# Performance work log

Hardware: AMD Instinct MI355X
Metric: run time of the kernel (lower is better)

Reference implementation:

```python
import jax, jax.numpy as jnp
import numpy as np

MODEL_DIM = 1024
H = 16
DK = MODEL_DIM // H


def setup_inputs() -> dict:
    key = jax.random.key(0)
    ks = jax.random.split(key, 11)
    B, S, D = 4, 2048, MODEL_DIM
    s = 1.0 / np.sqrt(D)
    inp = {
        "q": jax.random.normal(ks[0], (B, S, D), jnp.float32),
        "k": jax.random.normal(ks[1], (B, S, D), jnp.float32),
        "v": jax.random.normal(ks[2], (B, S, D), jnp.float32),
        # stacked per-head projection weights [H, D, DK] and biases [H, DK]
        "wq_w": jax.random.normal(ks[3], (H, D, DK), jnp.float32) * s,
        "wq_b": jax.random.normal(ks[4], (H, DK), jnp.float32) * s,
        "wk_w": jax.random.normal(ks[5], (H, D, DK), jnp.float32) * s,
        "wk_b": jax.random.normal(ks[6], (H, DK), jnp.float32) * s,
        "wv_w": jax.random.normal(ks[7], (H, D, DK), jnp.float32) * s,
        "wv_b": jax.random.normal(ks[8], (H, DK), jnp.float32) * s,
        "wo_w": jax.random.normal(ks[9], (D, D), jnp.float32) * s,
        "wo_b": jax.random.normal(ks[10], (D,), jnp.float32) * s,
    }
    return inp


def reference(q, k, v, wq_w, wq_b, wk_w, wk_b, wv_w, wv_b, wo_w, wo_b):
    # per-head projections, batched over heads: [B,S,D] x [H,D,DK] -> [B,H,S,DK]
    qh = jnp.einsum('bsd,hdk->bhsk', q, wq_w) + wq_b[None, :, None, :]
    kh = jnp.einsum('bsd,hdk->bhsk', k, wk_w) + wk_b[None, :, None, :]
    vh = jnp.einsum('bsd,hdk->bhsk', v, wv_w) + wv_b[None, :, None, :]
    scale = 1.0 / jnp.sqrt(jnp.asarray(DK, qh.dtype))
    scores = jnp.einsum('bhqk,bhsk->bhqs', qh, kh) * scale  # [B,H,S,S]
    out = jnp.einsum('bhqs,bhsk->bhqk', scores, vh)         # [B,H,S,DK]
    # NON-STANDARD: softmax applied AFTER the value matmul, over last dim (dv)
    out = jax.nn.softmax(out, axis=-1)
    # concat heads along feature dim: [B,S,H*DK]
    B, Hh, S, Dk = out.shape
    heads = jnp.transpose(out, (0, 2, 1, 3)).reshape(B, S, Hh * Dk)
    return heads @ wo_w.T + wo_b
```

## Files before the change

### kernel.cpp

```cpp
#include <hip/hip_runtime.h>
#include <math.h>

#define B 4
#define S 2048
#define D 1024
#define H 16
#define DK 64
#define MS (B * S)
#define GKA 2048

typedef short bf16x8 __attribute__((ext_vector_type(8)));
typedef float f32x4 __attribute__((ext_vector_type(4)));

__device__ __forceinline__ unsigned short f2bf(float x) {
  union { float f; unsigned u; } v; v.f = x;
  unsigned r = v.u + 0x7fff + ((v.u >> 16) & 1);
  return (unsigned short)(r >> 16);
}
__device__ __forceinline__ float bf2f(unsigned short h) {
  union { unsigned u; float f; } v; v.u = ((unsigned)h) << 16;
  return v.f;
}
__device__ __forceinline__ void split2(float x, unsigned short& hi, unsigned short& lo) {
  hi = f2bf(x);
  lo = f2bf(x - bf2f(hi));
}

__global__ __launch_bounds__(256) void prep_kernel(
    const float* __restrict__ q, const float* __restrict__ k, const float* __restrict__ v,
    const float* __restrict__ wk, const float* __restrict__ wv, const float* __restrict__ wq,
    const float* __restrict__ wo,
    unsigned short* __restrict__ KSP, unsigned short* __restrict__ VSP,
    unsigned short* __restrict__ QSP,
    unsigned short* __restrict__ WKS, unsigned short* __restrict__ WVS,
    unsigned short* __restrict__ WQA, unsigned short* __restrict__ WOB,
    float* __restrict__ M) {
  const int blk = blockIdx.x;
  const int tid = threadIdx.x;
  if (blk < 24576) {
    const int which = blk >> 13;
    const int bb = blk & 8191;
    const float* X = which == 0 ? k : (which == 1 ? v : q);
    unsigned short* O = which == 0 ? KSP : (which == 1 ? VSP : QSP);
    int t = bb * 256 + tid;
    int idx = t * 4;
    int m = idx >> 10, d = idx & 1023;
    float4 x = *(const float4*)&X[idx];
    union { unsigned short h[4]; ushort4 u; } uh, ul;
    split2(x.x, uh.h[0], ul.h[0]);
    split2(x.y, uh.h[1], ul.h[1]);
    split2(x.z, uh.h[2], ul.h[2]);
    split2(x.w, uh.h[3], ul.h[3]);
    *(ushort4*)&O[(size_t)m * GKA + d] = uh.u;
    *(ushort4*)&O[(size_t)m * GKA + 1024 + d] = ul.u;
  } else if (blk < 32768) {
    const int which = (blk - 24576) >> 12;
    const int bb = (blk - 24576) & 4095;
    const float* W = which == 0 ? wk : wv;
    unsigned short* O = which == 0 ? WKS : WVS;
    int t = bb * 256 + tid;
    int d = t & 1023, n = t >> 10;
    int h = n >> 6, dk = n & 63;
    float x = W[((size_t)(h << 10) + d) * 64 + dk];
    unsigned short hi, lo;
    split2(x, hi, lo);
    size_t ro = (size_t)n * GKA + d;
    O[ro] = hi;
    O[ro + 1024] = lo;
  } else if (blk < 36864) {
    int t = (blk - 32768) * 256 + tid;
    int kk = t & 63;
    int hd = t >> 6;
    float x = wq[t];
    unsigned short hi, lo;
    split2(x, hi, lo);
    WQA[(size_t)hd * 128 + kk] = hi;
    WQA[(size_t)hd * 128 + 64 + kk] = lo;
  } else if (blk < 37888) {
    int t = (blk - 36864) * 256 + tid;
    int idx = t * 4;
    float4 x = *(const float4*)&wo[idx];
    ushort4 u;
    u.x = f2bf(x.x); u.y = f2bf(x.y); u.z = f2bf(x.z); u.w = f2bf(x.w);
    *(ushort4*)&WOB[idx] = u;
  } else {
    int t = (blk - 37888) * 256 + tid;
    *(float4*)&M[(size_t)t * 4] = (float4){0.f, 0.f, 0.f, 0.f};
  }
}

#define BK 32
template <int SPLIT>
__global__ __launch_bounds__(256) void gemm_kernel(
    const unsigned short* __restrict__ A0, const unsigned short* __restrict__ A1,
    const unsigned short* __restrict__ B0, const unsigned short* __restrict__ B1,
    const float* __restrict__ bias0, const float* __restrict__ bias1,
    float* __restrict__ C0, float* __restrict__ C1) {
  const int KLOG = SPLIT ? 3072 : 1024;
  const int AST = SPLIT ? 2048 : 1024;
  const int BST = SPLIT ? 2048 : 1024;
  const unsigned short* A = blockIdx.z ? A1 : A0;
  const unsigned short* BT = blockIdx.z ? B1 : B0;
  const float* bias = blockIdx.z ? bias1 : bias0;
  float* C = blockIdx.z ? C1 : C0;

  __shared__ __align__(16) unsigned short As[128 * BK];
  __shared__ __align__(16) unsigned short Bs[128 * BK];
  const int tid = threadIdx.x;
  const int lane = tid & 63;
  const int w = tid >> 6;
  const int wm = (w >> 1) * 64;
  const int wn = (w & 1) * 64;
  const size_t bm = (size_t)blockIdx.y * 128;
  const size_t bn = (size_t)blockIdx.x * 128;

  f32x4 acc[4][4];
#pragma unroll
  for (int i = 0; i < 4; i++)
#pragma unroll
    for (int j = 0; j < 4; j++) acc[i][j] = (f32x4){0.f, 0.f, 0.f, 0.f};

  const int srow = lane >> 2;
  const int skof = (lane & 3) * 8;
  const unsigned short* Ag0 = A + (bm + w * 32 + srow) * AST + skof;
  const unsigned short* Ag1 = Ag0 + (size_t)16 * AST;
  const unsigned short* Bg0 = BT + (bn + w * 32 + srow) * BST + skof;
  const unsigned short* Bg1 = Bg0 + (size_t)16 * BST;
  unsigned short* As0 = As + (w * 2) * 512;
  unsigned short* As1 = As0 + 512;
  unsigned short* Bs0 = Bs + (w * 2) * 512;
  unsigned short* Bs1 = Bs0 + 512;

  const int fm = lane & 15;
  const int fk = (lane >> 4) * 8;

  for (int k0 = 0; k0 < KLOG; k0 += BK) {
    const int aofs = SPLIT ? (k0 < 2048 ? k0 : k0 - 2048) : k0;
    const int bofs = SPLIT ? (k0 < 1024 ? k0 : k0 - 1024) : k0;
    __syncthreads();
    __builtin_amdgcn_global_load_lds((const __attribute__((address_space(1))) void*)(Ag0 + aofs),
                                     (__attribute__((address_space(3))) void*)As0, 16, 0, 0);
    __builtin_amdgcn_global_load_lds((const __attribute__((address_space(1))) void*)(Ag1 + aofs),
                                     (__attribute__((address_space(3))) void*)As1, 16, 0, 0);
    __builtin_amdgcn_global_load_lds((const __attribute__((address_space(1))) void*)(Bg0 + bofs),
                                     (__attribute__((address_space(3))) void*)Bs0, 16, 0, 0);
    __builtin_amdgcn_global_load_lds((const __attribute__((address_space(1))) void*)(Bg1 + bofs),
                                     (__attribute__((address_space(3))) void*)Bs1, 16, 0, 0);
    __syncthreads();
    bf16x8 af[4], bf[4];
#pragma unroll
    for (int i = 0; i < 4; i++) {
      af[i] = *(const bf16x8*)&As[(wm + i * 16 + fm) * BK + fk];
      bf[i] = *(const bf16x8*)&Bs[(wn + i * 16 + fm) * BK + fk];
    }
#pragma unroll
    for (int i = 0; i < 4; i++)
#pragma unroll
      for (int j = 0; j < 4; j++)
        acc[i][j] = __builtin_amdgcn_mfma_f32_16x16x32_bf16(af[i], bf[j], acc[i][j], 0, 0, 0);
  }

  const int r0 = (lane >> 4) * 4;
#pragma unroll
  for (int i = 0; i < 4; i++)
#pragma unroll
    for (int j = 0; j < 4; j++) {
      size_t row = bm + wm + i * 16 + r0;
      size_t col = bn + wn + j * 16 + fm;
      float bb = bias[col];
#pragma unroll
      for (int r = 0; r < 4; r++) C[(row + r) * D + col] = acc[i][j][r] + bb;
    }
}

__global__ __launch_bounds__(256) void gemm_q_softmax(
    const unsigned short* __restrict__ A, const unsigned short* __restrict__ WQM,
    const float* __restrict__ BQM, unsigned short* __restrict__ HB) {
  const int b = blockIdx.y >> 4;
  const unsigned short* BT = WQM + (size_t)b * D * GKA;

  __shared__ __align__(16) unsigned short As[128 * BK];
  __shared__ __align__(16) unsigned short Bs[128 * BK];
  const int tid = threadIdx.x;
  const int lane = tid & 63;
  const int w = tid >> 6;
  const int wm = (w >> 1) * 64;
  const int wn = (w & 1) * 64;
  const size_t bm = (size_t)blockIdx.y * 128;
  const size_t bn = (size_t)blockIdx.x * 128;

  f32x4 acc[4][4];
#pragma unroll
  for (int i = 0; i < 4; i++)
#pragma unroll
    for (int j = 0; j < 4; j++) acc[i][j] = (f32x4){0.f, 0.f, 0.f, 0.f};

  const int srow = lane >> 2;
  const int skof = (lane & 3) * 8;
  const unsigned short* Ag0 = A + (bm + w * 32 + srow) * GKA + skof;
  const unsigned short* Ag1 = Ag0 + (size_t)16 * GKA;
  const unsigned short* Bg0 = BT + (bn + w * 32 + srow) * GKA + skof;
  const unsigned short* Bg1 = Bg0 + (size_t)16 * GKA;
  unsigned short* As0 = As + (w * 2) * 512;
  unsigned short* As1 = As0 + 512;
  unsigned short* Bs0 = Bs + (w * 2) * 512;
  unsigned short* Bs1 = Bs0 + 512;

  const int fm = lane & 15;
  const int fk = (lane >> 4) * 8;

  for (int k0 = 0; k0 < 3072; k0 += BK) {
    const int aofs = (k0 < 2048) ? k0 : k0 - 2048;
    const int bofs = (k0 < 1024) ? k0 : k0 - 1024;
    __syncthreads();
    __builtin_amdgcn_global_load_lds((const __attribute__((address_space(1))) void*)(Ag0 + aofs),
                                     (__attribute__((address_space(3))) void*)As0, 16, 0, 0);
    __builtin_amdgcn_global_load_lds((const __attribute__((address_space(1))) void*)(Ag1 + aofs),
                                     (__attribute__((address_space(3))) void*)As1, 16, 0, 0);
    __builtin_amdgcn_global_load_lds((const __attribute__((address_space(1))) void*)(Bg0 + bofs),
                                     (__attribute__((address_space(3))) void*)Bs0, 16, 0, 0);
    __builtin_amdgcn_global_load_lds((const __attribute__((address_space(1))) void*)(Bg1 + bofs),
                                     (__attribute__((address_space(3))) void*)Bs1, 16, 0, 0);
    __syncthreads();
    bf16x8 af[4], bf[4];
#pragma unroll
    for (int i = 0; i < 4; i++) {
      af[i] = *(const bf16x8*)&As[(wm + i * 16 + fm) * BK + fk];
      bf[i] = *(const bf16x8*)&Bs[(wn + i * 16 + fm) * BK + fk];
    }
#pragma unroll
    for (int i = 0; i < 4; i++)
#pragma unroll
      for (int j = 0; j < 4; j++)
        acc[i][j] = __builtin_amdgcn_mfma_f32_16x16x32_bf16(af[i], bf[j], acc[i][j], 0, 0, 0);
  }

  const int quad = lane >> 4;
  const size_t head_col0 = bn + wn;
  float bj[4];
#pragma unroll
  for (int j = 0; j < 4; j++) bj[j] = BQM[(size_t)b * D + head_col0 + j * 16 + fm];

#pragma unroll
  for (int i = 0; i < 4; i++) {
    f32x4 val[4];
#pragma unroll
    for (int j = 0; j < 4; j++)
#pragma unroll
      for (int r = 0; r < 4; r++) val[j][r] = (acc[i][j][r] + bj[j]) * 0.125f;

    f32x4 mx = val[0];
#pragma unroll
    for (int j = 1; j < 4; j++)
#pragma unroll
      for (int r = 0; r < 4; r++) mx[r] = fmaxf(mx[r], val[j][r]);
#pragma unroll
    for (int off = 1; off < 16; off <<= 1)
#pragma unroll
      for (int r = 0; r < 4; r++) mx[r] = fmaxf(mx[r], __shfl_xor(mx[r], off, 64));

    f32x4 e[4];
    f32x4 sm = (f32x4){0.f, 0.f, 0.f, 0.f};
#pragma unroll
    for (int j = 0; j < 4; j++)
#pragma unroll
      for (int r = 0; r < 4; r++) {
        e[j][r] = __expf(val[j][r] - mx[r]);
        sm[r] += e[j][r];
      }
#pragma unroll
    for (int off = 1; off < 16; off <<= 1)
#pragma unroll
      for (int r = 0; r < 4; r++) sm[r] += __shfl_xor(sm[r], off, 64);

    f32x4 inv;
#pragma unroll
    for (int r = 0; r < 4; r++) inv[r] = 1.0f / sm[r];

#pragma unroll
    for (int j = 0; j < 4; j++)
#pragma unroll
      for (int r = 0; r < 4; r++) {
        size_t row = bm + wm + i * 16 + quad * 4 + r;
        HB[row * D + head_col0 + j * 16 + fm] = f2bf(e[j][r] * inv[r]);
      }
  }
}

__global__ __launch_bounds__(256) void compute_m_kernel(
    const float* __restrict__ KH, const float* __restrict__ VH, float* __restrict__ Mout) {
  const int sc = blockIdx.x, h = blockIdx.y, b = blockIdx.z;
  const int tid = threadIdx.x;
  const int i0 = (tid >> 4) * 4;
  const int j0 = (tid & 15) * 4;
  __shared__ float ks[16][64], vs[16][64];
  float acc[4][4];
#pragma unroll
  for (int a = 0; a < 4; a++)
#pragma unroll
    for (int c = 0; c < 4; c++) acc[a][c] = 0.f;

  const int s0 = sc * (S / 8);
  const int rr = tid >> 4;
  const int cc = (tid & 15) * 4;
  for (int s = s0; s < s0 + S / 8; s += 16) {
    size_t base = ((size_t)b * S + s + rr) * D + h * 64 + cc;
    __syncthreads();
    *(float4*)&ks[rr][cc] = *(const float4*)&KH[base];
    *(float4*)&vs[rr][cc] = *(const float4*)&VH[base];
    __syncthreads();
#pragma unroll
    for (int ss = 0; ss < 16; ss++) {
      float4 kf = *(const float4*)&ks[ss][i0];
      float4 vf = *(const float4*)&vs[ss][j0];
      float ka[4] = {kf.x, kf.y, kf.z, kf.w};
      float va[4] = {vf.x, vf.y, vf.z, vf.w};
#pragma unroll
      for (int a = 0; a < 4; a++)
#pragma unroll
        for (int c = 0; c < 4; c++) acc[a][c] += ka[a] * va[c];
    }
  }
  float* Mp = Mout + ((size_t)(b * H + h)) * DK * DK;
#pragma unroll
  for (int a = 0; a < 4; a++)
#pragma unroll
    for (int c = 0; c < 4; c++) atomicAdd(&Mp[(i0 + a) * DK + j0 + c], acc[a][c]);
}

__global__ __launch_bounds__(256) void split_m_bias_kernel(
    const float* __restrict__ M, const float* __restrict__ bq,
    unsigned short* __restrict__ MSP, float* __restrict__ BQM) {
  const int bh = blockIdx.x;
  const int h = bh & 15;
  const float* Mp = M + (size_t)bh * 4096;
  unsigned short* hiP = MSP + (size_t)bh * 8192;
  unsigned short* loP = hiP + 4096;
  for (int idx = threadIdx.x; idx < 4096; idx += 256) {
    int kk = idx >> 6, nn = idx & 63;
    unsigned short hi, lo;
    split2(Mp[idx], hi, lo);
    hiP[nn * 64 + kk] = hi;
    loP[nn * 64 + kk] = lo;
  }
  if (threadIdx.x < 64) {
    int j = threadIdx.x;
    float a = 0.f;
#pragma unroll 8
    for (int kk = 0; kk < 64; kk++) a += bq[h * 64 + kk] * Mp[kk * 64 + j];
    BQM[(size_t)bh * 64 + j] = a;
  }
}

__global__ __launch_bounds__(256) void wqm_kernel(
    const unsigned short* __restrict__ WQA, const unsigned short* __restrict__ MSP,
    unsigned short* __restrict__ WQM) {
  const int c = blockIdx.x, h = blockIdx.y, b = blockIdx.z;
  const int tid = threadIdx.x;
  const int lane = tid & 63;
  const int w = tid >> 6;
  const int fm = lane & 15;
  const int quad = lane >> 4;
  const int ko = quad * 8;
  const int dbase = c * 64 + w * 16;

  const unsigned short* arow = WQA + ((size_t)h * 1024 + dbase + fm) * 128;
  bf16x8 ahi0 = *(const bf16x8*)&arow[ko];
  bf16x8 ahi1 = *(const bf16x8*)&arow[32 + ko];
  bf16x8 alo0 = *(const bf16x8*)&arow[64 + ko];
  bf16x8 alo1 = *(const bf16x8*)&arow[96 + ko];

  const unsigned short* hiP = MSP + ((size_t)(b * H + h)) * 8192;
  const unsigned short* loP = hiP + 4096;
  f32x4 acc[4];
#pragma unroll
  for (int j = 0; j < 4; j++) acc[j] = (f32x4){0.f, 0.f, 0.f, 0.f};
#pragma unroll
  for (int j = 0; j < 4; j++) {
    bf16x8 bhi0 = *(const bf16x8*)&hiP[(j * 16 + fm) * 64 + ko];
    bf16x8 bhi1 = *(const bf16x8*)&hiP[(j * 16 + fm) * 64 + 32 + ko];
    bf16x8 blo0 = *(const bf16x8*)&loP[(j * 16 + fm) * 64 + ko];
    bf16x8 blo1 = *(const bf16x8*)&loP[(j * 16 + fm) * 64 + 32 + ko];
    acc[j] = __builtin_amdgcn_mfma_f32_16x16x32_bf16(ahi0, bhi0, acc[j], 0, 0, 0);
    acc[j] = __builtin_amdgcn_mfma_f32_16x16x32_bf16(ahi1, bhi1, acc[j], 0, 0, 0);
    acc[j] = __builtin_amdgcn_mfma_f32_16x16x32_bf16(alo0, bhi0, acc[j], 0, 0, 0);
    acc[j] = __builtin_amdgcn_mfma_f32_16x16x32_bf16(alo1, bhi1, acc[j], 0, 0, 0);
    acc[j] = __builtin_amdgcn_mfma_f32_16x16x32_bf16(ahi0, blo0, acc[j], 0, 0, 0);
    acc[j] = __builtin_amdgcn_mfma_f32_16x16x32_bf16(ahi1, blo1, acc[j], 0, 0, 0);
  }

#pragma unroll
  for (int j = 0; j < 4; j++) {
    int n = h * 64 + j * 16 + fm;
    ushort4 hv, lv;
    unsigned short hi, lo;
    split2(acc[j][0], hi, lo); hv.x = hi; lv.x = lo;
    split2(acc[j][1], hi, lo); hv.y = hi; lv.y = lo;
    split2(acc[j][2], hi, lo); hv.z = hi; lv.z = lo;
    split2(acc[j][3], hi, lo); hv.w = hi; lv.w = lo;
    size_t base = ((size_t)b * D + n) * GKA + dbase + quad * 4;
    *(ushort4*)&WQM[base] = hv;
    *(ushort4*)&WQM[base + 1024] = lv;
  }
}

extern "C" void kernel_launch(void* const* d_in, const int* in_sizes, int n_in,
                              void* d_out, int out_size, void* d_ws, size_t ws_size,
                              hipStream_t stream) {
  const float* q = (const float*)d_in[0];
  const float* k = (const float*)d_in[1];
  const float* v = (const float*)d_in[2];
  const float* wq_w = (const float*)d_in[3];
  const float* wq_b = (const float*)d_in[4];
  const float* wk_w = (const float*)d_in[5];
  const float* wk_b = (const float*)d_in[6];
  const float* wv_w = (const float*)d_in[7];
  const float* wv_b = (const float*)d_in[8];
  const float* wo_w = (const float*)d_in[9];
  const float* wo_b = (const float*)d_in[10];
  float* out = (float*)d_out;

  unsigned short* KSP = (unsigned short*)d_ws;
  unsigned short* VSP = KSP + (size_t)16 * 1024 * 1024;
  unsigned short* QSP = VSP + (size_t)16 * 1024 * 1024;
  float* VH = (float*)(QSP + (size_t)16 * 1024 * 1024);
  float* M = VH + (size_t)MS * D;
  unsigned short* WKS = (unsigned short*)(M + 256 * 1024);
  unsigned short* WVS = WKS + (size_t)2 * 1024 * 1024;
  unsigned short* WQA = WVS + (size_t)2 * 1024 * 1024;
  unsigned short* WOB = WQA + (size_t)2 * 1024 * 1024;
  float* KH = out;
  unsigned short* HB = KSP;
  unsigned short* WQM = KSP + (size_t)8 * 1024 * 1024;
  unsigned short* MSP = VSP;
  float* BQM = (float*)(VSP + 512 * 1024);

  dim3 blk(256);

  prep_kernel<<<38144, blk, 0, stream>>>(q, k, v, wk_w, wv_w, wq_w, wo_w,
                                         KSP, VSP, QSP, WKS, WVS, WQA, WOB, M);
  gemm_kernel<1><<<dim3(8, 64, 2), blk, 0, stream>>>(KSP, VSP, WKS, WVS, wk_b, wv_b, KH, VH);
  compute_m_kernel<<<dim3(8, H, B), blk, 0, stream>>>(KH, VH, M);
  split_m_bias_kernel<<<64, blk, 0, stream>>>(M, wq_b, MSP, BQM);
  wqm_kernel<<<dim3(16, H, B), blk, 0, stream>>>(WQA, MSP, WQM);
  gemm_q_softmax<<<dim3(8, 64), blk, 0, stream>>>(QSP, WQM, BQM, HB);
  gemm_kernel<0><<<dim3(8, 64, 1), blk, 0, stream>>>(HB, HB, WOB, WOB, wo_b, wo_b, out, out);
}
```

Baseline: 480.7 us.

## Replace K/V projection GEMM with 256x256-tile double-buffered direct-to-LDS kernel

Adds a new GEMM kernel for the K and V projections that uses 256x256 output tiles with 512 threads. It double-buffers LDS staging through global_load_lds with an XOR swizzle to avoid bank conflicts, and raises wave priority around the MFMA blocks. The larger tile raises arithmetic intensity and the async loads overlap memory with compute, replacing the previous 128x128 gemm_kernel<1>. The trade-off is large LDS use (128KB per block) and high register pressure from 32 accumulators per lane, which limits occupancy. The 48-step K loop switches its source offset partway through, and that offset logic is easy to get wrong.

```diff
diff --git a/kernel.cpp b/kernel.cpp
--- a/kernel.cpp
+++ b/kernel.cpp
@@ -173,6 +173,126 @@
     }
 }
 
+__device__ __forceinline__ void stage256(
+    const unsigned short* __restrict__ A, const unsigned short* __restrict__ BT,
+    const unsigned* aoffs, const unsigned* boffs,
+    unsigned short* Asb, unsigned short* Bsb, int aof, int bof, int w) {
+#pragma unroll
+  for (int g = 0; g < 4; ++g)
+    __builtin_amdgcn_global_load_lds(
+        (const __attribute__((address_space(1))) void*)(A + aoffs[g] + aof),
+        (__attribute__((address_space(3))) void*)(Asb + g * 4096 + w * 512), 16, 0, 0);
+#pragma unroll
+  for (int g = 0; g < 4; ++g)
+    __builtin_amdgcn_global_load_lds(
+        (const __attribute__((address_space(1))) void*)(BT + boffs[g] + bof),
+        (__attribute__((address_space(3))) void*)(Bsb + g * 4096 + w * 512), 16, 0, 0);
+}
+
+__global__ __launch_bounds__(512, 2) void gemm256_kernel(
+    const unsigned short* __restrict__ A0, const unsigned short* __restrict__ A1,
+    const unsigned short* __restrict__ B0, const unsigned short* __restrict__ B1,
+    const float* __restrict__ bias0, const float* __restrict__ bias1,
+    float* __restrict__ C0, float* __restrict__ C1) {
+  const unsigned short* __restrict__ A = blockIdx.z ? A1 : A0;
+  const unsigned short* __restrict__ BT = blockIdx.z ? B1 : B0;
+  const float* __restrict__ bias = blockIdx.z ? bias1 : bias0;
+  float* __restrict__ C = blockIdx.z ? C1 : C0;
+
+  __shared__ __align__(16) unsigned short As[2][256 * 64];
+  __shared__ __align__(16) unsigned short Bs[2][256 * 64];
+
+  const int tid = threadIdx.x;
+  const int lane = tid & 63;
+  const int w = tid >> 6;
+  const int wr = w >> 2;
+  const int wc = w & 3;
+  const int fm = lane & 15;
+  const int quad = lane >> 4;
+  const int sx = (fm & 7) << 3;
+  const size_t bm = (size_t)blockIdx.y * 256;
+  const size_t bn = (size_t)blockIdx.x * 256;
+
+  const int srow = tid >> 3;
+  const int scol = ((tid & 7) ^ (srow & 7)) << 3;
+  unsigned aoffs[4], boffs[4];
+#pragma unroll
+  for (int g = 0; g < 4; ++g) {
+    aoffs[g] = (unsigned)((bm + g * 64 + srow) * 2048 + scol);
+    boffs[g] = (unsigned)((bn + g * 64 + srow) * 2048 + scol);
+  }
+
+  f32x4 acc[8][4];
+#pragma unroll
+  for (int i = 0; i < 8; ++i)
+#pragma unroll
+    for (int j = 0; j < 4; ++j) acc[i][j] = (f32x4){0.f, 0.f, 0.f, 0.f};
+
+  stage256(A, BT, aoffs, boffs, As[0], Bs[0], 0, 0, w);
+  stage256(A, BT, aoffs, boffs, As[1], Bs[1], 64, 64, w);
+
+  for (int t = 0; t < 48; ++t) {
+    const int cur = t & 1;
+    if (t < 47)
+      asm volatile("s_waitcnt vmcnt(8)" ::: "memory");
+    else
+      asm volatile("s_waitcnt vmcnt(0)" ::: "memory");
+    __builtin_amdgcn_s_barrier();
+    asm volatile("" ::: "memory");
+
+    const unsigned short* Ab = As[cur];
+    const unsigned short* Bb = Bs[cur];
+
+    bf16x8 bfr[4][2];
+#pragma unroll
+    for (int j = 0; j < 4; ++j)
+#pragma unroll
+      for (int kk = 0; kk < 2; ++kk)
+        bfr[j][kk] = *(const bf16x8*)&Bb[((wc * 64 + j * 16 + fm) * 64 + kk * 32 + quad * 8) ^ sx];
+
+#pragma unroll
+    for (int qq = 0; qq < 4; ++qq) {
+      bf16x8 afr[2][2];
+#pragma unroll
+      for (int ii = 0; ii < 2; ++ii)
+#pragma unroll
+        for (int kk = 0; kk < 2; ++kk)
+          afr[ii][kk] = *(const bf16x8*)&Ab[((wr * 128 + (qq * 2 + ii) * 16 + fm) * 64 + kk * 32 + quad * 8) ^ sx];
+      __builtin_amdgcn_s_setprio(1);
+#pragma unroll
+      for (int ii = 0; ii < 2; ++ii)
+#pragma unroll
+        for (int j = 0; j < 4; ++j) {
+          acc[qq * 2 + ii][j] =
+              __builtin_amdgcn_mfma_f32_16x16x32_bf16(afr[ii][0], bfr[j][0], acc[qq * 2 + ii][j], 0, 0, 0);
+          acc[qq * 2 + ii][j] =
+              __builtin_amdgcn_mfma_f32_16x16x32_bf16(afr[ii][1], bfr[j][1], acc[qq * 2 + ii][j], 0, 0, 0);
+        }
+      __builtin_amdgcn_s_setprio(0);
+      __builtin_amdgcn_s_barrier();
+      asm volatile("" ::: "memory");
+    }
+
+    if (t + 2 < 48) {
+      const int k0 = (t + 2) * 64;
+      const int aof = k0 < 2048 ? k0 : k0 - 2048;
+      const int bof = k0 < 1024 ? k0 : k0 - 1024;
+      stage256(A, BT, aoffs, boffs, As[cur], Bs[cur], aof, bof, w);
+    }
+  }
+
+#pragma unroll
+  for (int i = 0; i < 8; ++i)
+#pragma unroll
+    for (int j = 0; j < 4; ++j) {
+      size_t row = bm + wr * 128 + i * 16 + quad * 4;
+      size_t col = bn + wc * 64 + j * 16 + fm;
+      float bb = bias[col];
+#pragma unroll
+      for (int r = 0; r < 4; ++r) C[(row + r) * D + col] = acc[i][j][r] + bb;
+    }
+}
+
 __global__ __launch_bounds__(256) void gemm_q_softmax(
     const unsigned short* __restrict__ A, const unsigned short* __restrict__ WQM,
     const float* __restrict__ BQM, unsigned short* __restrict__ HB) {
@@ -439,7 +559,7 @@
 
   prep_kernel<<<38144, blk, 0, stream>>>(q, k, v, wk_w, wv_w, wq_w, wo_w,
                                          KSP, VSP, QSP, WKS, WVS, WQA, WOB, M);
-  gemm_kernel<1><<<dim3(8, 64, 2), blk, 0, stream>>>(KSP, VSP, WKS, WVS, wk_b, wv_b, KH, VH);
+  gemm256_kernel<<<dim3(4, 32, 2), dim3(512), 0, stream>>>(KSP, VSP, WKS, WVS, wk_b, wv_b, KH, VH);
   compute_m_kernel<<<dim3(8, H, B), blk, 0, stream>>>(KH, VH, M);
   split_m_bias_kernel<<<64, blk, 0, stream>>>(M, wq_b, MSP, BQM);
   wqm_kernel<<<dim3(16, H, B), blk, 0, stream>>>(WQA, MSP, WQM);
```

After: 465.3 us. -3.2%, faster.

## Replace GEMMs with 256-row double-buffered swizzled-LDS MFMA kernel

Applied to the files above, without the earlier changes.

Replaces the three 128x128 single-stage GEMM kernels with one templated 512-thread kernel using 256-row tiles, BK=64, and two LDS buffers. The next k-tile loads asynchronously while the current one is computed, with explicit vmcnt/lgkmcnt waits and priority hints. An XOR swizzle on LDS addresses is meant to avoid bank conflicts. This aims to hide global-memory latency and raise MFMA utilization, at the cost of more LDS per block and fewer blocks in the grid.

```diff
diff --git a/kernel.cpp b/kernel.cpp
--- a/kernel.cpp
+++ b/kernel.cpp
@@ -89,201 +89,210 @@
   }
 }
 
-#define BK 32
-template <int SPLIT>
-__global__ __launch_bounds__(256) void gemm_kernel(
+__device__ __forceinline__ void gll(const unsigned short* g, unsigned short* l) {
+  __builtin_amdgcn_global_load_lds((const __attribute__((address_space(1))) void*)g,
+                                   (__attribute__((address_space(3))) void*)l, 16, 0, 0);
+}
+
+template <int NWC, int EPI, int KLOG>
+__global__ __launch_bounds__(512, 2) void gemm256(
     const unsigned short* __restrict__ A0, const unsigned short* __restrict__ A1,
-    const unsigned short* __restrict__ B0, const unsigned short* __restrict__ B1,
+    const unsigned short* __restrict__ Bt0, const unsigned short* __restrict__ Bt1,
     const float* __restrict__ bias0, const float* __restrict__ bias1,
-    float* __restrict__ C0, float* __restrict__ C1) {
-  const int KLOG = SPLIT ? 3072 : 1024;
-  const int AST = SPLIT ? 2048 : 1024;
-  const int BST = SPLIT ? 2048 : 1024;
-  const unsigned short* A = blockIdx.z ? A1 : A0;
-  const unsigned short* BT = blockIdx.z ? B1 : B0;
-  const float* bias = blockIdx.z ? bias1 : bias0;
-  float* C = blockIdx.z ? C1 : C0;
-
-  __shared__ __align__(16) unsigned short As[128 * BK];
-  __shared__ __align__(16) unsigned short Bs[128 * BK];
+    void* __restrict__ C0, void* __restrict__ C1) {
+  constexpr int NWR = 8 / NWC;
+  constexpr int MR = (256 / NWR) / 16;
+  constexpr int BN = NWC * 64;
+  constexpr int AST = (KLOG == 1024) ? 1024 : 2048;
+  constexpr int NKT = KLOG / 64;
+  constexpr int LPS = 4 + NWC;
+
+  __shared__ __align__(16) unsigned short As[2][256 * 64];
+  __shared__ __align__(16) unsigned short Bs[2][BN * 64];
+
   const int tid = threadIdx.x;
   const int lane = tid & 63;
   const int w = tid >> 6;
-  const int wm = (w >> 1) * 64;
-  const int wn = (w & 1) * 64;
-  const size_t bm = (size_t)blockIdx.y * 128;
-  const size_t bn = (size_t)blockIdx.x * 128;
-
-  f32x4 acc[4][4];
-#pragma unroll
-  for (int i = 0; i < 4; i++)
-#pragma unroll
-    for (int j = 0; j < 4; j++) acc[i][j] = (f32x4){0.f, 0.f, 0.f, 0.f};
-
-  const int srow = lane >> 2;
-  const int skof = (lane & 3) * 8;
-  const unsigned short* Ag0 = A + (bm + w * 32 + srow) * AST + skof;
-  const unsigned short* Ag1 = Ag0 + (size_t)16 * AST;
-  const unsigned short* Bg0 = BT + (bn + w * 32 + srow) * BST + skof;
-  const unsigned short* Bg1 = Bg0 + (size_t)16 * BST;
-  unsigned short* As0 = As + (w * 2) * 512;
-  unsigned short* As1 = As0 + 512;
-  unsigned short* Bs0 = Bs + (w * 2) * 512;
-  unsigned short* Bs1 = Bs0 + 512;
-
+  const int wr = w / NWC;
+  const int wc = w % NWC;
   const int fm = lane & 15;
-  const int fk = (lane >> 4) * 8;
-
-  for (int k0 = 0; k0 < KLOG; k0 += BK) {
-    const int aofs = SPLIT ? (k0 < 2048 ? k0 : k0 - 2048) : k0;
-    const int bofs = SPLIT ? (k0 < 1024 ? k0 : k0 - 1024) : k0;
-    __syncthreads();
-    __builtin_amdgcn_global_load_lds((const __attribute__((address_space(1))) void*)(Ag0 + aofs),
-                                     (__attribute__((address_space(3))) void*)As0, 16, 0, 0);
-    __builtin_amdgcn_global_load_lds((const __attribute__((address_space(1))) void*)(Ag1 + aofs),
-                                     (__attribute__((address_space(3))) void*)As1, 16, 0, 0);
-    __builtin_amdgcn_global_load_lds((const __attribute__((address_space(1))) void*)(Bg0 + bofs),
-                                     (__attribute__((address_space(3))) void*)Bs0, 16, 0, 0);
-    __builtin_amdgcn_global_load_lds((const __attribute__((address_space(1))) void*)(Bg1 + bofs),
-                                     (__attribute__((address_space(3))) void*)Bs1, 16, 0, 0);
-    __syncthreads();
-    bf16x8 af[4], bf[4];
-#pragma unroll
-    for (int i = 0; i < 4; i++) {
-      af[i] = *(const bf16x8*)&As[(wm + i * 16 + fm) * BK + fk];
-      bf[i] = *(const bf16x8*)&Bs[(wn + i * 16 + fm) * BK + fk];
+  const int quad = lane >> 4;
+  const int sx = (fm & 7) << 3;
+  const size_t bm = (size_t)blockIdx.y * 256;
+  const size_t bn = (size_t)blockIdx.x * BN;
+
+  const unsigned short* A;
+  const unsigned short* BT;
+  const float* bias;
+  if constexpr (EPI == 1) {
+    const int b = blockIdx.y >> 3;
+    A = A0;
+    BT = Bt0 + (size_t)b * D * GKA;
+    bias = bias0 + (size_t)b * D;
+  } else {
+    A = blockIdx.z ? A1 : A0;
+    BT = blockIdx.z ? Bt1 : Bt0;
+    bias = blockIdx.z ? bias1 : bias0;
+  }
+
+  const int srow = tid >> 3;
+  const int scol = ((tid & 7) ^ (srow & 7)) << 3;
+  unsigned aoffs[4], boffs[NWC];
+#pragma unroll
+  for (int g = 0; g < 4; ++g) aoffs[g] = (unsigned)((bm + g * 64 + srow) * AST + scol);
+#pragma unroll
+  for (int g = 0; g < NWC; ++g) boffs[g] = (unsigned)((bn + g * 64 + srow) * AST + scol);
+
+  int bidx[4][2], aidx[MR][2];
+#pragma unroll
+  for (int j = 0; j < 4; ++j)
+#pragma unroll
+    for (int kk = 0; kk < 2; ++kk)
+      bidx[j][kk] = ((wc * 64 + j * 16 + fm) * 64 + kk * 32 + quad * 8) ^ sx;
+#pragma unroll
+  for (int i = 0; i < MR; ++i)
+#pragma unroll
+    for (int kk = 0; kk < 2; ++kk)
+      aidx[i][kk] = ((wr * (MR * 16) + i * 16 + fm) * 64 + kk * 32 + quad * 8) ^ sx;
+
+  f32x4 acc[MR][4];
+#pragma unroll
+  for (int i = 0; i < MR; ++i)
+#pragma unroll
+    for (int j = 0; j < 4; ++j) acc[i][j] = (f32x4){0.f, 0.f, 0.f, 0.f};
+
+  auto koff_a = [](int k0) { return (KLOG == 3072) ? (k0 < 2048 ? k0 : k0 - 2048) : k0; };
+  auto koff_b = [](int k0) { return (KLOG == 3072) ? (k0 < 1024 ? k0 : k0 - 1024) : k0; };
+
+  auto stage = [&](unsigned short* Asb, unsigned short* Bsb, int aof, int bof) {
+#pragma unroll
+    for (int g = 0; g < 4; ++g) gll(A + aoffs[g] + aof, Asb + g * 4096 + w * 512);
+#pragma unroll
+    for (int g = 0; g < NWC; ++g) gll(BT + boffs[g] + bof, Bsb + g * 4096 + w * 512);
+  };
+
+  stage(As[0], Bs[0], koff_a(0), koff_b(0));
+  stage(As[1], Bs[1], koff_a(64), koff_b(64));
+
+  auto tile = [&](const unsigned short* Ab, const unsigned short* Bb,
+                  unsigned short* Asb, unsigned short* Bsb, int t) {
+    if (t < NKT - 1) {
+      if constexpr (NWC == 4) asm volatile("s_waitcnt vmcnt(8)" ::: "memory");
+      else                    asm volatile("s_waitcnt vmcnt(6)" ::: "memory");
+    } else {
+      asm volatile("s_waitcnt vmcnt(0)" ::: "memory");
     }
-#pragma unroll
-    for (int i = 0; i < 4; i++)
-#pragma unroll
-      for (int j = 0; j < 4; j++)
-        acc[i][j] = __builtin_amdgcn_mfma_f32_16x16x32_bf16(af[i], bf[j], acc[i][j], 0, 0, 0);
-  }
-
-  const int r0 = (lane >> 4) * 4;
-#pragma unroll
-  for (int i = 0; i < 4; i++)
-#pragma unroll
-    for (int j = 0; j < 4; j++) {
-      size_t row = bm + wm + i * 16 + r0;
-      size_t col = bn + wn + j * 16 + fm;
-      float bb = bias[col];
-#pragma unroll
-      for (int r = 0; r < 4; r++) C[(row + r) * D + col] = acc[i][j][r] + bb;
+    __builtin_amdgcn_s_barrier();
+    __builtin_amdgcn_sched_barrier(0);
+
+    bf16x8 b0f[4], a0f[MR], b1f[4], a1f[MR];
+#pragma unroll
+    for (int j = 0; j < 4; ++j) b0f[j] = *(const bf16x8*)&Bb[bidx[j][0]];
+#pragma unroll
+    for (int i = 0; i < MR; ++i) a0f[i] = *(const bf16x8*)&Ab[aidx[i][0]];
+    __builtin_amdgcn_sched_barrier(0);
+#pragma unroll
+    for (int j = 0; j < 4; ++j) b1f[j] = *(const bf16x8*)&Bb[bidx[j][1]];
+#pragma unroll
+    for (int i = 0; i < MR; ++i) a1f[i] = *(const bf16x8*)&Ab[aidx[i][1]];
+    if constexpr (NWC == 4) asm volatile("s_waitcnt lgkmcnt(12)" ::: "memory");
+    else                    asm volatile("s_waitcnt lgkmcnt(8)" ::: "memory");
+    __builtin_amdgcn_sched_barrier(0);
+
+    __builtin_amdgcn_s_setprio(1);
+#pragma unroll
+    for (int i = 0; i < MR; ++i)
+#pragma unroll
+      for (int j = 0; j < 4; ++j)
+        acc[i][j] = __builtin_amdgcn_mfma_f32_16x16x32_bf16(a0f[i], b0f[j], acc[i][j], 0, 0, 0);
+    __builtin_amdgcn_s_setprio(0);
+
+    asm volatile("s_waitcnt lgkmcnt(0)" ::: "memory");
+    __builtin_amdgcn_sched_barrier(0);
+    __builtin_amdgcn_s_barrier();
+    if (t + 2 < NKT) {
+      const int k0 = (t + 2) * 64;
+      stage(Asb, Bsb, koff_a(k0), koff_b(k0));
     }
-}
-
-__global__ __launch_bounds__(256) void gemm_q_softmax(
-    const unsigned short* __restrict__ A, const unsigned short* __restrict__ WQM,
-    const float* __restrict__ BQM, unsigned short* __restrict__ HB) {
-  const int b = blockIdx.y >> 4;
-  const unsigned short* BT = WQM + (size_t)b * D * GKA;
-
-  __shared__ __align__(16) unsigned short As[128 * BK];
-  __shared__ __align__(16) unsigned short Bs[128 * BK];
-  const int tid = threadIdx.x;
-  const int lane = tid & 63;
-  const int w = tid >> 6;
-  const int wm = (w >> 1) * 64;
-  const int wn = (w & 1) * 64;
-  const size_t bm = (size_t)blockIdx.y * 128;
-  const size_t bn = (size_t)blockIdx.x * 128;
-
-  f32x4 acc[4][4];
-#pragma unroll
-  for (int i = 0; i < 4; i++)
-#pragma unroll
-    for (int j = 0; j < 4; j++) acc[i][j] = (f32x4){0.f, 0.f, 0.f, 0.f};
-
-  const int srow = lane >> 2;
-  const int skof = (lane & 3) * 8;
-  const unsigned short* Ag0 = A + (bm + w * 32 + srow) * GKA + skof;
-  const unsigned short* Ag1 = Ag0 + (size_t)16 * GKA;
-  const unsigned short* Bg0 = BT + (bn + w * 32 + srow) * GKA + skof;
-  const unsigned short* Bg1 = Bg0 + (size_t)16 * GKA;
-  unsigned short* As0 = As + (w * 2) * 512;
-  unsigned short* As1 = As0 + 512;
-  unsigned short* Bs0 = Bs + (w * 2) * 512;
-  unsigned short* Bs1 = Bs0 + 512;
-
-  const int fm = lane & 15;
-  const int fk = (lane >> 4) * 8;
-
-  for (int k0 = 0; k0 < 3072; k0 += BK) {
-    const int aofs = (k0 < 2048) ? k0 : k0 - 2048;
-    const int bofs = (k0 < 1024) ? k0 : k0 - 1024;
-    __syncthreads();
-    __builtin_amdgcn_global_load_lds((const __attribute__((address_space(1))) void*)(Ag0 + aofs),
-                                     (__attribute__((address_space(3))) void*)As0, 16, 0, 0);
-    __builtin_amdgcn_global_load_lds((const __attribute__((address_space(1))) void*)(Ag1 + aofs),
-                                     (__attribute__((address_space(3))) void*)As1, 16, 0, 0);
-    __builtin_amdgcn_global_load_lds((const __attribute__((address_space(1))) void*)(Bg0 + bofs),
-                                     (__attribute__((address_space(3))) void*)Bs0, 16, 0, 0);
-    __builtin_amdgcn_global_load_lds((const __attribute__((address_space(1))) void*)(Bg1 + bofs),
-                                     (__attribute__((address_space(3))) void*)Bs1, 16, 0, 0);
-    __syncthreads();
-    bf16x8 af[4], bf[4];
-#pragma unroll
-    for (int i = 0; i < 4; i++) {
-      af[i] = *(const bf16x8*)&As[(wm + i * 16 + fm) * BK + fk];
-      bf[i] = *(const bf16x8*)&Bs[(wn + i * 16 + fm) * BK + fk];
+    __builtin_amdgcn_sched_barrier(0);
+
+    __builtin_amdgcn_s_setprio(1);
+#pragma unroll
+    for (int i = 0; i < MR; ++i)
+#pragma unroll
+      for (int j = 0; j < 4; ++j)
+        acc[i][j] = __builtin_amdgcn_mfma_f32_16x16x32_bf16(a1f[i], b1f[j], acc[i][j], 0, 0, 0);
+    __builtin_amdgcn_s_setprio(0);
+  };
+
+#pragma unroll 1
+  for (int tp = 0; tp < NKT / 2; ++tp) {
+    tile(As[0], Bs[0], As[0], Bs[0], 2 * tp);
+    tile(As[1], Bs[1], As[1], Bs[1], 2 * tp + 1);
+  }
+
+  if constexpr (EPI == 0) {
+    float* C = (float*)(blockIdx.z ? C1 : C0);
+#pragma unroll
+    for (int i = 0; i < MR; ++i)
+#pragma unroll
+      for (int j = 0; j < 4; ++j) {
+        size_t row = bm + wr * (MR * 16) + i * 16 + quad * 4;
+        size_t col = bn + wc * 64 + j * 16 + fm;
+        float bb = bias[col];
+#pragma unroll
+        for (int r = 0; r < 4; ++r) C[(row + r) * D + col] = acc[i][j][r] + bb;
+      }
+  } else {
+    unsigned short* HB = (unsigned short*)C0;
+    const size_t head_col0 = bn + wc * 64;
+    float bj[4];
+#pragma unroll
+    for (int j = 0; j < 4; ++j) bj[j] = bias[head_col0 + j * 16 + fm];
+#pragma unroll
+    for (int i = 0; i < MR; ++i) {
+      f32x4 val[4];
+#pragma unroll
+      for (int j = 0; j < 4; ++j)
+#pragma unroll
+        for (int r = 0; r < 4; ++r) val[j][r] = (acc[i][j][r] + bj[j]) * 0.125f;
+
+      f32x4 mx = val[0];
+#pragma unroll
+      for (int j = 1; j < 4; ++j)
+#pragma unroll
+        for (int r = 0; r < 4; ++r) mx[r] = fmaxf(mx[r], val[j][r]);
+#pragma unroll
+      for (int off = 1; off < 16; off <<= 1)
+#pragma unroll
+        for (int r = 0; r < 4; ++r) mx[r] = fmaxf(mx[r], __shfl_xor(mx[r], off, 64));
+
+      f32x4 e[4];
+      f32x4 sm = (f32x4){0.f, 0.f, 0.f, 0.f};
+#pragma unroll
+      for (int j = 0; j < 4; ++j)
+#pragma unroll
+        for (int r = 0; r < 4; ++r) {
+          e[j][r] = __expf(val[j][r] - mx[r]);
+          sm[r] += e[j][r];
+        }
+#pragma unroll
+      for (int off = 1; off < 16; off <<= 1)
+#pragma unroll
+        for (int r = 0; r < 4; ++r) sm[r] += __shfl_xor(sm[r], off, 64);
+
+      f32x4 inv;
+#pragma unroll
+      for (int r = 0; r < 4; ++r) inv[r] = 1.0f / sm[r];
+
+#pragma unroll
+      for (int j = 0; j < 4; ++j)
+#pragma unroll
+        for (int r = 0; r < 4; ++r) {
+          size_t row = bm + wr * (MR * 16) + i * 16 + quad * 4 + r;
+          HB[row * D + head_col0 + j * 16 + fm] = f2bf(e[j][r] * inv[r]);
+        }
     }
-#pragma unroll
-    for (int i = 0; i < 4; i++)
-#pragma unroll
-      for (int j = 0; j < 4; j++)
-        acc[i][j] = __builtin_amdgcn_mfma_f32_16x16x32_bf16(af[i], bf[j], acc[i][j], 0, 0, 0);
-  }
-
-  const int quad = lane >> 4;
-  const size_t head_col0 = bn + wn;
-  float bj[4];
-#pragma unroll
-  for (int j = 0; j < 4; j++) bj[j] = BQM[(size_t)b * D + head_col0 + j * 16 + fm];
-
-#pragma unroll
-  for (int i = 0; i < 4; i++) {
-    f32x4 val[4];
-#pragma unroll
-    for (int j = 0; j < 4; j++)
-#pragma unroll
-      for (int r = 0; r < 4; r++) val[j][r] = (acc[i][j][r] + bj[j]) * 0.125f;
-
-    f32x4 mx = val[0];
-#pragma unroll
-    for (int j = 1; j < 4; j++)
-#pragma unroll
-      for (int r = 0; r < 4; r++) mx[r] = fmaxf(mx[r], val[j][r]);
-#pragma unroll
-    for (int off = 1; off < 16; off <<= 1)
-#pragma unroll
-      for (int r = 0; r < 4; r++) mx[r] = fmaxf(mx[r], __shfl_xor(mx[r], off, 64));
-
-    f32x4 e[4];
-    f32x4 sm = (f32x4){0.f, 0.f, 0.f, 0.f};
-#pragma unroll
-    for (int j = 0; j < 4; j++)
-#pragma unroll
-      for (int r = 0; r < 4; r++) {
-        e[j][r] = __expf(val[j][r] - mx[r]);
-        sm[r] += e[j][r];
-      }
-#pragma unroll
-    for (int off = 1; off < 16; off <<= 1)
-#pragma unroll
-      for (int r = 0; r < 4; r++) sm[r] += __shfl_xor(sm[r], off, 64);
-
-    f32x4 inv;
-#pragma unroll
-    for (int r = 0; r < 4; r++) inv[r] = 1.0f / sm[r];
-
-#pragma unroll
-    for (int j = 0; j < 4; j++)
-#pragma unroll
-      for (int r = 0; r < 4; r++) {
-        size_t row = bm + wm + i * 16 + quad * 4 + r;
-        HB[row * D + head_col0 + j * 16 + fm] = f2bf(e[j][r] * inv[r]);
-      }
   }
 }
 
@@ -439,10 +448,13 @@
 
   prep_kernel<<<38144, blk, 0, stream>>>(q, k, v, wk_w, wv_w, wq_w, wo_w,
                                          KSP, VSP, QSP, WKS, WVS, WQA, WOB, M);
-  gemm_kernel<1><<<dim3(8, 64, 2), blk, 0, stream>>>(KSP, VSP, WKS, WVS, wk_b, wv_b, KH, VH);
+  gemm256<4, 0, 3072><<<dim3(4, 32, 2), dim3(512), 0, stream>>>(
+      KSP, VSP, WKS, WVS, wk_b, wv_b, KH, VH);
   compute_m_kernel<<<dim3(8, H, B), blk, 0, stream>>>(KH, VH, M);
   split_m_bias_kernel<<<64, blk, 0, stream>>>(M, wq_b, MSP, BQM);
   wqm_kernel<<<dim3(16, H, B), blk, 0, stream>>>(WQA, MSP, WQM);
-  gemm_q_softmax<<<dim3(8, 64), blk, 0, stream>>>(QSP, WQM, BQM, HB);
-  gemm_kernel<0><<<dim3(8, 64, 1), blk, 0, stream>>>(HB, HB, WOB, WOB, wo_b, wo_b, out, out);
-}
+  gemm256<2, 1, 3072><<<dim3(8, 32, 1), dim3(512), 0, stream>>>(
+      QSP, nullptr, WQM, nullptr, BQM, nullptr, HB, nullptr);
+  gemm256<2, 0, 1024><<<dim3(8, 32, 1), dim3(512), 0, stream>>>(
+      HB, HB, WOB, WOB, wo_b, wo_b, out, out);
+}
```

Result: slower. 753.9 us (+56.8%).
